# Kernel optimization log

Hardware: AMD Instinct MI355X
Metric: run time of the kernel (lower is better)

Reference implementation:

```python
import jax, jax.numpy as jnp
import numpy as np

NEG_SLOPE = 0.2
CLAMP = 1e9

C, N, T, IN_F = 8, 1024, 3, 64
H, OUT_F = 4, 64
E = 65536


def setup_inputs() -> dict:
    key = jax.random.key(0)
    k1, k2, k3, k4, k5 = jax.random.split(key, 5)
    edge_idx = jax.random.randint(k1, (2, E), 0, C * N, dtype=jnp.int64)
    node_feats = jax.random.normal(k2, (C, N, T, IN_F), dtype=jnp.float32)
    # xavier-ish scaling for parameters
    fc = jax.random.normal(k3, (T, IN_F, OUT_F * H), dtype=jnp.float32) * (2.0 / (IN_F + OUT_F * H)) ** 0.5
    attn_src = jax.random.normal(k4, (1, H, OUT_F * T), dtype=jnp.float32) * 0.1
    attn_dst = jax.random.normal(k5, (1, H, OUT_F * T), dtype=jnp.float32) * 0.1
    return {"edge_idx": edge_idx, "node_feats": node_feats, "fc": fc,
            "attn_src": attn_src, "attn_dst": attn_dst}


def reference(edge_idx, node_feats, fc, attn_src, attn_dst):
    c, n, t, f_in = node_feats.shape
    h = attn_src.shape[1]
    f_out = fc.shape[2] // h
    cn = c * n

    # per-node-type linear transform: (cn, t, in) x (t, in, h*out) -> (cn, t, h*out)
    hs = node_feats.reshape(cn, t, f_in)
    feat = jnp.einsum('bji,jik->bjk', hs, fc)

    # replicate the torch permute/reshape sequence exactly (row-major reshapes)
    x = feat.reshape(c, n, t, f_out * h)
    x = jnp.transpose(x, (0, 2, 1, 3))                  # (c, t, n, h*out)
    x = x.reshape(c, n, t, h, f_out)                    # torch .reshape on permuted copy
    x = jnp.transpose(x, (0, 1, 3, 2, 4))               # (c, n, h, t, out)
    feat_flat = x.reshape(cn, h, t * f_out)             # feat_src = feat_dst

    # node masks from edge endpoints (scatter 1s on rows)
    msrc = jnp.zeros((cn,), node_feats.dtype).at[edge_idx[0]].set(1.0)
    mdst = jnp.zeros((cn,), node_feats.dtype).at[edge_idx[1]].set(1.0)
    feat_src = feat_flat * msrc[:, None, None]
    feat_dst = feat_flat * mdst[:, None, None]

    a_src = jnp.clip(feat_src * attn_src, -CLAMP, CLAMP).reshape(c, n, h, f_out * t).sum(-1)
    a_dst = jnp.clip(feat_dst * attn_dst, -CLAMP, CLAMP).reshape(c, n, h, f_out * t).sum(-1)

    a = a_src[:, :, None, :] + a_dst[:, None, :, :]     # (c, n, n, h)
    a = jnp.where(a >= 0, a, NEG_SLOPE * a)             # leaky relu
    a = jnp.clip(a, -CLAMP, CLAMP)
    a = jax.nn.softmax(a, axis=0)                       # softmax over conformers (dim=0, as in source)

    fd = feat_dst.reshape(c, n, h, t * f_out)
    m = jnp.einsum('cvuh,cuhf->cvhf', a, fd)            # (c, n, h, t*out)
    m = jax.nn.relu(m)
    outs = m.reshape(c, n, h, t, f_out).sum(axis=2)     # (c, n, t, out)
    return outs, a
```

## Files before the change

kernel.cpp:

```cpp
#include <hip/hip_runtime.h>
#include <stdint.h>

#define CC 8
#define NN 1024
#define CN 8192
#define NE 65536
#define NEG_SLOPE 0.2f

typedef __attribute__((ext_vector_type(8))) short bf16x8;
typedef __attribute__((ext_vector_type(4))) float f32x4;

__device__ __forceinline__ ushort f2bfu(float x) {
    unsigned u = __float_as_uint(x);
    unsigned r = u + 0x7fffu + ((u >> 16) & 1u);
    return (ushort)(r >> 16);
}

__global__ void k_scatter(const int* __restrict__ edges,
                          float* __restrict__ msrc, float* __restrict__ mdst) {
    int e = blockIdx.x * 256 + threadIdx.x;
    if (e < NE) {
        msrc[edges[e]] = 1.0f;
        mdst[edges[NE + e]] = 1.0f;
    }
}

__global__ void __launch_bounds__(256) k_feat(const float* __restrict__ nf,
                                              const float* __restrict__ fc,
                                              float* __restrict__ feat) {
    __shared__ float sFC[64][132];
    __shared__ float sHT[64][36];
    int t = threadIdx.x;
    int tt = blockIdx.y;
    int kh = blockIdx.x & 1;
    int r0 = (blockIdx.x >> 1) * 32;
    {
        const float* fcp = fc + tt * 16384 + kh * 128;
        #pragma unroll
        for (int i = 0; i < 8; ++i) {
            int f4 = t + 256 * i;
            int row = f4 >> 5, c4 = f4 & 31;
            *(float4*)&sFC[row][c4 * 4] = *(const float4*)(fcp + row * 256 + c4 * 4);
        }
    }
    {
        #pragma unroll
        for (int i = 0; i < 2; ++i) {
            int f4 = t + 256 * i;
            int r = f4 >> 4, c4 = f4 & 15;
            float4 v = *(const float4*)(nf + (size_t)(r0 + r) * 192 + tt * 64 + c4 * 4);
            sHT[c4 * 4 + 0][r] = v.x;
            sHT[c4 * 4 + 1][r] = v.y;
            sHT[c4 * 4 + 2][r] = v.z;
            sHT[c4 * 4 + 3][r] = v.w;
        }
    }
    __syncthreads();
    int rg = t >> 5;
    int kg = t & 31;
    float acc[4][4];
    #pragma unroll
    for (int a = 0; a < 4; ++a)
        #pragma unroll
        for (int b = 0; b < 4; ++b) acc[a][b] = 0.f;
    #pragma unroll 4
    for (int i = 0; i < 64; ++i) {
        float4 hv = *(const float4*)&sHT[i][rg * 4];
        float4 fv = *(const float4*)&sFC[i][kg * 4];
        const float* fp = (const float*)&fv;
        #pragma unroll
        for (int b = 0; b < 4; ++b) {
            acc[0][b] += hv.x * fp[b];
            acc[1][b] += hv.y * fp[b];
            acc[2][b] += hv.z * fp[b];
            acc[3][b] += hv.w * fp[b];
        }
    }
    #pragma unroll
    for (int a = 0; a < 4; ++a) {
        int b = r0 + rg * 4 + a;
        int c = b >> 10, n = b & 1023;
        float4 vv = {acc[a][0], acc[a][1], acc[a][2], acc[a][3]};
        *(float4*)(feat + (size_t)c * 786432 + (size_t)tt * 262144 + n * 256 + kh * 128 + kg * 4) = vv;
    }
}

__global__ void __launch_bounds__(256) k_rt(const float* __restrict__ feat,
                        const float* __restrict__ attn_src, const float* __restrict__ attn_dst,
                        const float* __restrict__ msrc, const float* __restrict__ mdst,
                        ushort* __restrict__ fdt, float* __restrict__ a_src, float* __restrict__ a_dst) {
    __shared__ ushort T[22560];
    int u0 = blockIdx.x * 64;
    int t2 = blockIdx.y;
    int c  = blockIdx.z;
    int t = threadIdx.x;
    int nl = t >> 2, q = t & 3;
    int b = (c << 10) + u0 + nl;
    float md = mdst[b], ms = msrc[b];
    const float* fp  = feat + (size_t)c * 786432 + (size_t)(u0 + nl) * 768 + t2 * 256 + q * 64;
    const float* wsp = attn_src + q * 192 + t2 * 64;
    const float* wdp = attn_dst + q * 192 + t2 * 64;
    float ssum = 0.f, dsum = 0.f;
    #pragma unroll
    for (int i4 = 0; i4 < 16; ++i4) {
        float4 v = *(const float4*)(fp + i4 * 4);
        const float* vv = (const float*)&v;
        #pragma unroll
        for (int k = 0; k < 4; ++k) {
            int f = i4 * 4 + k;
            ssum += vv[k] * wsp[f];
            dsum += vv[k] * wdp[f];
            T[(q * 64 + f) * 88 + q * 16 + nl] = f2bfu(vv[k] * md);
        }
    }
    atomicAdd(&a_src[(b << 2) + q], ssum * ms);
    atomicAdd(&a_dst[(b << 2) + q], dsum * md);
    __syncthreads();
    int h2 = t >> 6, j = t & 63;
    const ushort* row = &T[(h2 * 64 + j) * 88 + h2 * 16];
    ushort* dst = fdt + (size_t)((c * 4 + h2) * 192 + t2 * 64 + j) * 1024 + u0;
    #pragma unroll
    for (int i = 0; i < 8; ++i)
        *(uint4*)(dst + i * 8) = *(const uint4*)(row + i * 8);
}

__global__ void __launch_bounds__(256) k_att(const float* __restrict__ a_src,
                                             const float* __restrict__ a_dst,
                                             float* __restrict__ a_out, ushort* __restrict__ Abuf) {
    __shared__ float sAS[32];
    int v = blockIdx.x;
    int t = threadIdx.x;
    if (t < 32) sAS[t] = a_src[((t >> 2) * 1024 + v) * 4 + (t & 3)];
    __syncthreads();
    int u0 = blockIdx.y * 512 + t * 2;

    float mx0[4], mx1[4];
    #pragma unroll
    for (int h = 0; h < 4; ++h) { mx0[h] = -1e30f; mx1[h] = -1e30f; }
    #pragma unroll
    for (int c = 0; c < 8; ++c) {
        float4 d0 = *(const float4*)(a_dst + ((c << 10) + u0) * 4);
        float4 d1 = *(const float4*)(a_dst + ((c << 10) + u0 + 1) * 4);
        const float* dp0 = (const float*)&d0;
        const float* dp1 = (const float*)&d1;
        #pragma unroll
        for (int h = 0; h < 4; ++h) {
            float as = sAS[c * 4 + h];
            mx0[h] = fmaxf(mx0[h], as + dp0[h]);
            mx1[h] = fmaxf(mx1[h], as + dp1[h]);
        }
    }
    #pragma unroll
    for (int h = 0; h < 4; ++h) {
        float x = mx0[h];
        x = (x >= 0.f) ? x : NEG_SLOPE * x;
        mx0[h] = fminf(fmaxf(x, -1e9f), 1e9f);
        float y = mx1[h];
        y = (y >= 0.f) ? y : NEG_SLOPE * y;
        mx1[h] = fminf(fmaxf(y, -1e9f), 1e9f);
    }

    float s0[4] = {0.f, 0.f, 0.f, 0.f}, s1[4] = {0.f, 0.f, 0.f, 0.f};
    #pragma unroll
    for (int c = 0; c < 8; ++c) {
        float4 d0 = *(const float4*)(a_dst + ((c << 10) + u0) * 4);
        float4 d1 = *(const float4*)(a_dst + ((c << 10) + u0 + 1) * 4);
        const float* dp0 = (const float*)&d0;
        const float* dp1 = (const float*)&d1;
        #pragma unroll
        for (int h = 0; h < 4; ++h) {
            float as = sAS[c * 4 + h];
            float x = as + dp0[h];
            x = (x >= 0.f) ? x : NEG_SLOPE * x;
            x = fminf(fmaxf(x, -1e9f), 1e9f);
            s0[h] += __expf(x - mx0[h]);
            float y = as + dp1[h];
            y = (y >= 0.f) ? y : NEG_SLOPE * y;
            y = fminf(fmaxf(y, -1e9f), 1e9f);
            s1[h] += __expf(y - mx1[h]);
        }
    }
    float r0[4], r1[4];
    #pragma unroll
    for (int h = 0; h < 4; ++h) { r0[h] = 1.f / s0[h]; r1[h] = 1.f / s1[h]; }

    #pragma unroll
    for (int c = 0; c < 8; ++c) {
        float4 d0 = *(const float4*)(a_dst + ((c << 10) + u0) * 4);
        float4 d1 = *(const float4*)(a_dst + ((c << 10) + u0 + 1) * 4);
        const float* dp0 = (const float*)&d0;
        const float* dp1 = (const float*)&d1;
        float w0[4], w1[4];
        unsigned packs[4];
        #pragma unroll
        for (int h = 0; h < 4; ++h) {
            float as = sAS[c * 4 + h];
            float x = as + dp0[h];
            x = (x >= 0.f) ? x : NEG_SLOPE * x;
            x = fminf(fmaxf(x, -1e9f), 1e9f);
            float p0 = __expf(x - mx0[h]) * r0[h];
            float y = as + dp1[h];
            y = (y >= 0.f) ? y : NEG_SLOPE * y;
            y = fminf(fmaxf(y, -1e9f), 1e9f);
            float p1 = __expf(y - mx1[h]) * r1[h];
            w0[h] = p0; w1[h] = p1;
            packs[h] = (unsigned)f2bfu(p0) | ((unsigned)f2bfu(p1) << 16);
        }
        float* ao = a_out + ((size_t)((c << 10) + v) * 1024 + u0) * 4;
        *(float4*)ao = *(const float4*)w0;
        *((float4*)ao + 1) = *(const float4*)w1;
        #pragma unroll
        for (int h = 0; h < 4; ++h)
            *(unsigned*)(Abuf + (size_t)((c * 4 + h) * 1024 + v) * 1024 + u0) = packs[h];
    }
}

__global__ void __launch_bounds__(256) k_gemm(const ushort* __restrict__ A,
                                              const ushort* __restrict__ B,
                                              float* __restrict__ Mout) {
    __shared__ ushort sA[64 * 72];
    __shared__ ushort sB[192 * 72];
    int ch = blockIdx.y;
    int v0 = blockIdx.x * 64;
    int t = threadIdx.x;
    const ushort* pA = A + (size_t)ch * (1024 * 1024) + (size_t)v0 * 1024;
    const ushort* pB = B + (size_t)ch * (192 * 1024);
    int wid = t >> 6, lane = t & 63;
    int wn = wid * 48;
    int lm = lane & 15, lq = lane >> 4;
    f32x4 acc[4][3];
    #pragma unroll
    for (int i = 0; i < 4; ++i)
        #pragma unroll
        for (int j = 0; j < 3; ++j)
            acc[i][j] = (f32x4){0.f, 0.f, 0.f, 0.f};
    for (int kk = 0; kk < 1024; kk += 64) {
        #pragma unroll
        for (int i = 0; i < 2; ++i) {
            int cid = t + 256 * i;
            int r = cid >> 3, kc = cid & 7;
            uint4 vv = *(const uint4*)(pA + (size_t)r * 1024 + kk + kc * 8);
            *(uint4*)&sA[r * 72 + kc * 8] = vv;
        }
        #pragma unroll
        for (int i = 0; i < 6; ++i) {
            int cid = t + 256 * i;
            int r = cid >> 3, kc = cid & 7;
            uint4 vv = *(const uint4*)(pB + (size_t)r * 1024 + kk + kc * 8);
            *(uint4*)&sB[r * 72 + kc * 8] = vv;
        }
        __syncthreads();
        #pragma unroll
        for (int ks = 0; ks < 64; ks += 32) {
            bf16x8 af[4], bg[3];
            #pragma unroll
            for (int i = 0; i < 4; ++i)
                af[i] = *(const bf16x8*)&sA[(i * 16 + lm) * 72 + ks + lq * 8];
            #pragma unroll
            for (int j = 0; j < 3; ++j)
                bg[j] = *(const bf16x8*)&sB[(wn + j * 16 + lm) * 72 + ks + lq * 8];
            #pragma unroll
            for (int i = 0; i < 4; ++i)
                #pragma unroll
                for (int j = 0; j < 3; ++j)
                    acc[i][j] = __builtin_amdgcn_mfma_f32_16x16x32_bf16(af[i], bg[j], acc[i][j], 0, 0, 0);
        }
        __syncthreads();
    }
    float* pM = Mout + (size_t)ch * 196608 + (size_t)v0 * 192;
    #pragma unroll
    for (int i = 0; i < 4; ++i)
        #pragma unroll
        for (int r = 0; r < 4; ++r) {
            int row = i * 16 + lq * 4 + r;
            #pragma unroll
            for (int j = 0; j < 3; ++j)
                pM[(size_t)row * 192 + wn + j * 16 + lm] = acc[i][j][r];
        }
}

__global__ void k_out(const float* __restrict__ Mm, float* __restrict__ outp) {
    int b = blockIdx.x;
    int c = b >> 10, v = b & 1023;
    int tf = threadIdx.x;
    float s = 0.f;
    #pragma unroll
    for (int h = 0; h < 4; ++h) {
        float x = Mm[(size_t)(c * 4 + h) * 196608 + (size_t)v * 192 + tf];
        s += fmaxf(x, 0.f);
    }
    outp[(size_t)b * 192 + tf] = s;
}

extern "C" void kernel_launch(void* const* d_in, const int* in_sizes, int n_in,
                              void* d_out, int out_size, void* d_ws, size_t ws_size,
                              hipStream_t stream) {
    const int*   edges  = (const int*)d_in[0];
    const float* nf     = (const float*)d_in[1];
    const float* fc     = (const float*)d_in[2];
    const float* asrc_w = (const float*)d_in[3];
    const float* adst_w = (const float*)d_in[4];
    float* outp  = (float*)d_out;
    float* a_out = outp + 1572864;

    char* ws = (char*)d_ws;
    float*  msrc  = (float*)(ws + 0);
    float*  mdst  = (float*)(ws + 32768);
    float*  a_src = (float*)(ws + 65536);
    float*  a_dst = (float*)(ws + 196608);
    ushort* fdt   = (ushort*)(ws + 327680);
    float*  feat  = (float*)(ws + 12910592);
    float*  Mm    = feat;
    ushort* Abuf  = (ushort*)(ws + 38076416);

    hipMemsetAsync(msrc, 0, 327680, stream);
    k_scatter<<<dim3(256), dim3(256), 0, stream>>>(edges, msrc, mdst);
    k_feat<<<dim3(512, 3), dim3(256), 0, stream>>>(nf, fc, feat);
    k_rt<<<dim3(16, 3, 8), dim3(256), 0, stream>>>(feat, asrc_w, adst_w, msrc, mdst, fdt, a_src, a_dst);
    k_att<<<dim3(1024, 2), dim3(256), 0, stream>>>(a_src, a_dst, a_out, Abuf);
    k_gemm<<<dim3(16, 32), dim3(256), 0, stream>>>(Abuf, fdt, Mm);
    k_out<<<dim3(8192), dim3(192), 0, stream>>>(Mm, outp);
}
```

Baseline: 287.9 us.

## Coalesce attention writes and double GEMM row tile with 512-thread blocks

In the attention kernel each thread now handles columns u and u+256 rather than two adjacent columns. Wavefront stores of the float4 attention output are therefore contiguous, at the cost of 2-byte rather than 4-byte bf16 stores to Abuf. The GEMM now uses 128-row tiles with 8 waves in a 2x4 layout, so each B tile loaded into shared memory serves twice as many rows. This halves grid size to 256 blocks and raises shared memory per block.

New measurement: 254.9 us. -11.5%, faster.

```diff
diff --git a/kernel.cpp b/kernel.cpp
--- a/kernel.cpp
+++ b/kernel.cpp
@@ -132,7 +132,8 @@
     int t = threadIdx.x;
     if (t < 32) sAS[t] = a_src[((t >> 2) * 1024 + v) * 4 + (t & 3)];
     __syncthreads();
-    int u0 = blockIdx.y * 512 + t * 2;
+    int u0 = blockIdx.y * 512 + t;
+    int u1 = u0 + 256;
 
     float mx0[4], mx1[4];
     #pragma unroll
@@ -140,7 +141,7 @@
     #pragma unroll
     for (int c = 0; c < 8; ++c) {
         float4 d0 = *(const float4*)(a_dst + ((c << 10) + u0) * 4);
-        float4 d1 = *(const float4*)(a_dst + ((c << 10) + u0 + 1) * 4);
+        float4 d1 = *(const float4*)(a_dst + ((c << 10) + u1) * 4);
         const float* dp0 = (const float*)&d0;
         const float* dp1 = (const float*)&d1;
         #pragma unroll
@@ -164,7 +165,7 @@
     #pragma unroll
     for (int c = 0; c < 8; ++c) {
         float4 d0 = *(const float4*)(a_dst + ((c << 10) + u0) * 4);
-        float4 d1 = *(const float4*)(a_dst + ((c << 10) + u0 + 1) * 4);
+        float4 d1 = *(const float4*)(a_dst + ((c << 10) + u1) * 4);
         const float* dp0 = (const float*)&d0;
         const float* dp1 = (const float*)&d1;
         #pragma unroll
@@ -187,46 +188,47 @@
     #pragma unroll
     for (int c = 0; c < 8; ++c) {
         float4 d0 = *(const float4*)(a_dst + ((c << 10) + u0) * 4);
-        float4 d1 = *(const float4*)(a_dst + ((c << 10) + u0 + 1) * 4);
+        float4 d1 = *(const float4*)(a_dst + ((c << 10) + u1) * 4);
         const float* dp0 = (const float*)&d0;
         const float* dp1 = (const float*)&d1;
         float w0[4], w1[4];
-        unsigned packs[4];
         #pragma unroll
         for (int h = 0; h < 4; ++h) {
             float as = sAS[c * 4 + h];
             float x = as + dp0[h];
             x = (x >= 0.f) ? x : NEG_SLOPE * x;
             x = fminf(fmaxf(x, -1e9f), 1e9f);
-            float p0 = __expf(x - mx0[h]) * r0[h];
+            w0[h] = __expf(x - mx0[h]) * r0[h];
             float y = as + dp1[h];
             y = (y >= 0.f) ? y : NEG_SLOPE * y;
             y = fminf(fmaxf(y, -1e9f), 1e9f);
-            float p1 = __expf(y - mx1[h]) * r1[h];
-            w0[h] = p0; w1[h] = p1;
-            packs[h] = (unsigned)f2bfu(p0) | ((unsigned)f2bfu(p1) << 16);
-        }
-        float* ao = a_out + ((size_t)((c << 10) + v) * 1024 + u0) * 4;
-        *(float4*)ao = *(const float4*)w0;
-        *((float4*)ao + 1) = *(const float4*)w1;
-        #pragma unroll
-        for (int h = 0; h < 4; ++h)
-            *(unsigned*)(Abuf + (size_t)((c * 4 + h) * 1024 + v) * 1024 + u0) = packs[h];
-    }
-}
-
-__global__ void __launch_bounds__(256) k_gemm(const ushort* __restrict__ A,
+            w1[h] = __expf(y - mx1[h]) * r1[h];
+        }
+        float* ao0 = a_out + ((size_t)((c << 10) + v) * 1024 + u0) * 4;
+        float* ao1 = a_out + ((size_t)((c << 10) + v) * 1024 + u1) * 4;
+        *(float4*)ao0 = *(const float4*)w0;
+        *(float4*)ao1 = *(const float4*)w1;
+        #pragma unroll
+        for (int h = 0; h < 4; ++h) {
+            ushort* ab = Abuf + (size_t)((c * 4 + h) * 1024 + v) * 1024;
+            ab[u0] = f2bfu(w0[h]);
+            ab[u1] = f2bfu(w1[h]);
+        }
+    }
+}
+
+__global__ void __launch_bounds__(512) k_gemm(const ushort* __restrict__ A,
                                               const ushort* __restrict__ B,
                                               float* __restrict__ Mout) {
-    __shared__ ushort sA[64 * 72];
+    __shared__ ushort sA[128 * 72];
     __shared__ ushort sB[192 * 72];
     int ch = blockIdx.y;
-    int v0 = blockIdx.x * 64;
+    int v0 = blockIdx.x * 128;
     int t = threadIdx.x;
     const ushort* pA = A + (size_t)ch * (1024 * 1024) + (size_t)v0 * 1024;
     const ushort* pB = B + (size_t)ch * (192 * 1024);
     int wid = t >> 6, lane = t & 63;
-    int wn = wid * 48;
+    int wm = (wid >> 2) * 64, wn = (wid & 3) * 48;
     int lm = lane & 15, lq = lane >> 4;
     f32x4 acc[4][3];
     #pragma unroll
@@ -237,14 +239,14 @@
     for (int kk = 0; kk < 1024; kk += 64) {
         #pragma unroll
         for (int i = 0; i < 2; ++i) {
-            int cid = t + 256 * i;
+            int cid = t + 512 * i;
             int r = cid >> 3, kc = cid & 7;
             uint4 vv = *(const uint4*)(pA + (size_t)r * 1024 + kk + kc * 8);
             *(uint4*)&sA[r * 72 + kc * 8] = vv;
         }
         #pragma unroll
-        for (int i = 0; i < 6; ++i) {
-            int cid = t + 256 * i;
+        for (int i = 0; i < 3; ++i) {
+            int cid = t + 512 * i;
             int r = cid >> 3, kc = cid & 7;
             uint4 vv = *(const uint4*)(pB + (size_t)r * 1024 + kk + kc * 8);
             *(uint4*)&sB[r * 72 + kc * 8] = vv;
@@ -255,7 +257,7 @@
             bf16x8 af[4], bg[3];
             #pragma unroll
             for (int i = 0; i < 4; ++i)
-                af[i] = *(const bf16x8*)&sA[(i * 16 + lm) * 72 + ks + lq * 8];
+                af[i] = *(const bf16x8*)&sA[(wm + i * 16 + lm) * 72 + ks + lq * 8];
             #pragma unroll
             for (int j = 0; j < 3; ++j)
                 bg[j] = *(const bf16x8*)&sB[(wn + j * 16 + lm) * 72 + ks + lq * 8];
@@ -272,7 +274,7 @@
     for (int i = 0; i < 4; ++i)
         #pragma unroll
         for (int r = 0; r < 4; ++r) {
-            int row = i * 16 + lq * 4 + r;
+            int row = wm + i * 16 + lq * 4 + r;
             #pragma unroll
             for (int j = 0; j < 3; ++j)
                 pM[(size_t)row * 192 + wn + j * 16 + lm] = acc[i][j][r];
@@ -318,6 +320,6 @@
     k_feat<<<dim3(512, 3), dim3(256), 0, stream>>>(nf, fc, feat);
     k_rt<<<dim3(16, 3, 8), dim3(256), 0, stream>>>(feat, asrc_w, adst_w, msrc, mdst, fdt, a_src, a_dst);
     k_att<<<dim3(1024, 2), dim3(256), 0, stream>>>(a_src, a_dst, a_out, Abuf);
-    k_gemm<<<dim3(16, 32), dim3(256), 0, stream>>>(Abuf, fdt, Mm);
+    k_gemm<<<dim3(8, 32), dim3(512), 0, stream>>>(Abuf, fdt, Mm);
     k_out<<<dim3(8192), dim3(192), 0, stream>>>(Mm, outp);
 }
```
